# Kernel tuning notes

Hardware: AMD Instinct MI355X
Metric: run time of the kernel (lower is better)

The kernel has to match this reference:

```python
import jax, jax.numpy as jnp
import numpy as np

N_VARS = 100
MAX_LAG = 10
HIDDEN = 64
E = N_VARS * MAX_LAG  # number of tiny expert MLPs
BATCH = 4096


def setup_inputs() -> dict:
    key = jax.random.key(0)
    k_x, k_w1, k_b1, k_w2, k_b2 = jax.random.split(key, 5)
    x = jax.random.normal(k_x, (BATCH, E), dtype=jnp.float32)
    # PyTorch Linear(1, H): weight [H,1] -> stacked as [E, H]; bias [E, H]
    lim1 = 1.0  # kaiming-uniform-ish bound for fan_in=1
    W1 = jax.random.uniform(k_w1, (E, HIDDEN), dtype=jnp.float32, minval=-lim1, maxval=lim1)
    b1 = jax.random.uniform(k_b1, (E, HIDDEN), dtype=jnp.float32, minval=-lim1, maxval=lim1)
    # Linear(H, n_vars): weight [n_vars,H] -> stacked as [E, H, n_vars]; bias [E, n_vars]
    lim2 = 1.0 / np.sqrt(HIDDEN)
    W2 = jax.random.uniform(k_w2, (E, HIDDEN, N_VARS), dtype=jnp.float32, minval=-lim2, maxval=lim2)
    b2 = jax.random.uniform(k_b2, (E, N_VARS), dtype=jnp.float32, minval=-lim2, maxval=lim2)
    return {"x": x, "W1": W1, "b1": b1, "W2": W2, "b2": b2}


def reference(x, W1, b1, W2, b2):
    # Fused form of: sum_i Linear2_i(relu(Linear1_i(x[:, i:i+1])))
    # h[b,e,h] = relu(x[b,e] * W1[e,h] + b1[e,h])
    h = jax.nn.relu(x[:, :, None] * W1[None, :, :] + b1[None, :, :])  # [B,E,H]
    # sum over experts folded into the contraction: out[b,v] = sum_e h[b,e,:] @ W2[e,:,v]
    out = jnp.einsum("beh,ehv->bv", h, W2) + jnp.sum(b2, axis=0)  # [B,n_vars]
    return out
```

## Files before the change

kernel.cpp:

```cpp
#include <hip/hip_runtime.h>
#include <hip/hip_bf16.h>

#define NV 100
#define HID 64
#define NE 1000
#define NB 4096
#define ESPLIT 32
#define W2E 3584

typedef __attribute__((ext_vector_type(8))) short short8;
typedef __attribute__((ext_vector_type(4))) float f32x4;

__device__ __align__(16) float g_bsum[NV];

__device__ __forceinline__ short cvtbf(float f) {
    return __builtin_bit_cast(short, (__bf16)f);
}
__device__ __forceinline__ unsigned short f2bf(float f) {
    return (unsigned short)__builtin_bit_cast(short, (__bf16)f);
}
__device__ __forceinline__ float bf2f(unsigned short s) {
    union { unsigned u; float f; } v; v.u = ((unsigned)s) << 16;
    return v.f;
}
__device__ __forceinline__ unsigned pkbf(float a, float b) {
    return (unsigned)f2bf(a) | ((unsigned)f2bf(b) << 16);
}

__device__ __host__ __forceinline__ void esplit_range(int ks, int* pe0, int* pne) {
    int e0 = (ks < 26) ? 32 * ks : 832 + 28 * (ks - 26);
    int ne = (ks < 26) ? 32 : 28;
    *pe0 = e0; *pne = ne;
}

__global__ void bias_kernel(const float* __restrict__ b2) {
    int v = blockIdx.x;
    float s = 0.f;
    for (int e = threadIdx.x; e < NE; e += 256)
        s += b2[e * NV + v];
    __shared__ float red[4];
    for (int off = 32; off; off >>= 1) s += __shfl_down(s, off, 64);
    if ((threadIdx.x & 63) == 0) red[threadIdx.x >> 6] = s;
    __syncthreads();
    if (threadIdx.x == 0) g_bsum[v] = red[0] + red[1] + red[2] + red[3];
}

__global__ void init_kernel(float* __restrict__ out) {
    int idx = blockIdx.x * 256 + threadIdx.x;
    if (idx < NB * NV) out[idx] = g_bsum[idx % NV];
}

__global__ void prepass3(const float* __restrict__ W2, unsigned* __restrict__ w2bf) {
    __shared__ float t[HID][NV + 1];
    int e = blockIdx.x;
    const float* src = W2 + (size_t)e * (HID * NV);
    for (int i = threadIdx.x; i < HID * NV; i += 256) {
        int hh = i / NV;
        int v = i - hh * NV;
        t[hh][v] = src[i];
    }
    __syncthreads();
    unsigned* dst = w2bf + (size_t)e * W2E;
    for (int o = threadIdx.x; o < W2E; o += 256) {
        int f = o >> 8;
        int r = o & 255;
        int l = r >> 2;
        int q = r & 3;
        int ksh = f / 7, tt = f - 7 * ksh;
        int kg = l >> 4, lrow = l & 15;
        int h0 = ksh * 32 + kg * 8 + 2 * q;
        int v = tt * 16 + lrow;
        unsigned val = 0;
        if (v < NV) val = pkbf(t[h0][v], t[h0 + 1][v]);
        dst[o] = val;
    }
}

__global__ __launch_bounds__(256, 2) void moe5(
    const float* __restrict__ x, const float* __restrict__ W1,
    const float* __restrict__ b1, const unsigned* __restrict__ w2bf,
    float* __restrict__ part)
{
    __shared__ __align__(16) unsigned char smem[61440];
    unsigned short* xts = (unsigned short*)(smem + 28672);
    float* w1l = (float*)(smem + 45056);
    float* b1l = (float*)(smem + 53248);

    const int bid = blockIdx.x;
    const int xcd = bid & 7;
    const int jj  = bid >> 3;
    const int ks  = xcd * 4 + (jj & 3);
    const int mb  = jj >> 2;

    const int tid  = threadIdx.x;
    const int lane = tid & 63;
    const int wave = tid >> 6;
    const int lrow = lane & 15;
    const int kg   = lane >> 4;

    const int row0 = mb * 256;
    int e0, ne; esplit_range(ks, &e0, &ne);

    {
        const float* xp = x + (size_t)(row0 + tid) * NE + e0;
        #pragma unroll
        for (int c4 = 0; c4 < 8; ++c4) {
            int eb = c4 * 4;
            if (eb < ne) {
                float4 v = *(const float4*)(xp + eb);
                xts[(eb + 0) * 256 + tid] = f2bf(v.x);
                xts[(eb + 1) * 256 + tid] = f2bf(v.y);
                xts[(eb + 2) * 256 + tid] = f2bf(v.z);
                xts[(eb + 3) * 256 + tid] = f2bf(v.w);
            }
        }
    }
    {
        int e = tid >> 3;
        int h = (tid & 7) * 8;
        if (e < ne) {
            const float* wsrc = W1 + (size_t)(e0 + e) * HID + h;
            const float* bsrc = b1 + (size_t)(e0 + e) * HID + h;
            *(float4*)&w1l[e * 64 + h]     = *(const float4*)(wsrc);
            *(float4*)&w1l[e * 64 + h + 4] = *(const float4*)(wsrc + 4);
            *(float4*)&b1l[e * 64 + h]     = *(const float4*)(bsrc);
            *(float4*)&b1l[e * 64 + h + 4] = *(const float4*)(bsrc + 4);
        }
    }

    auto stage_w2 = [&](int buf, int e) {
        const unsigned* g = w2bf + (size_t)e * W2E;
        unsigned* lbase = (unsigned*)(smem + buf * 14336);
        #pragma unroll
        for (int k = 0; k < 3; ++k) {
            int off16 = k * 256 + tid;
            __builtin_amdgcn_global_load_lds(
                (const __attribute__((address_space(1))) unsigned*)(g + off16 * 4),
                (__attribute__((address_space(3))) unsigned*)(lbase + off16 * 4),
                16, 0, 0);
        }
        if (tid < 128)
            __builtin_amdgcn_global_load_lds(
                (const __attribute__((address_space(1))) unsigned*)(g + (768 + tid) * 4),
                (__attribute__((address_space(3))) unsigned*)(lbase + (768 + tid) * 4),
                16, 0, 0);
    };

    stage_w2(0, e0);
    __syncthreads();

    f32x4 acc[4][7];
    #pragma unroll
    for (int rf = 0; rf < 4; ++rf)
        #pragma unroll
        for (int t = 0; t < 7; ++t)
            acc[rf][t] = (f32x4){0.f, 0.f, 0.f, 0.f};

    int cur = 0;
    for (int ei = 0; ei < ne; ++ei) {
        if (ei + 1 < ne) stage_w2(cur ^ 1, e0 + ei + 1);

        float xv[4];
        #pragma unroll
        for (int rf = 0; rf < 4; ++rf)
            xv[rf] = bf2f(xts[ei * 256 + wave * 64 + rf * 16 + lrow]);

        const unsigned char* w2c = smem + cur * 14336 + lane * 16;

        #pragma unroll
        for (int ksh = 0; ksh < 2; ++ksh) {
            const int hb = ksh * 32 + kg * 8;
            float4 wa = *(const float4*)&w1l[ei * 64 + hb];
            float4 wb = *(const float4*)&w1l[ei * 64 + hb + 4];
            float4 ba = *(const float4*)&b1l[ei * 64 + hb];
            float4 bb = *(const float4*)&b1l[ei * 64 + hb + 4];

            short8 afr[4];
            #pragma unroll
            for (int rf = 0; rf < 4; ++rf) {
                float xr = xv[rf];
                short8 a;
                a[0] = cvtbf(fmaxf(fmaf(xr, wa.x, ba.x), 0.f));
                a[1] = cvtbf(fmaxf(fmaf(xr, wa.y, ba.y), 0.f));
                a[2] = cvtbf(fmaxf(fmaf(xr, wa.z, ba.z), 0.f));
                a[3] = cvtbf(fmaxf(fmaf(xr, wa.w, ba.w), 0.f));
                a[4] = cvtbf(fmaxf(fmaf(xr, wb.x, bb.x), 0.f));
                a[5] = cvtbf(fmaxf(fmaf(xr, wb.y, bb.y), 0.f));
                a[6] = cvtbf(fmaxf(fmaf(xr, wb.z, bb.z), 0.f));
                a[7] = cvtbf(fmaxf(fmaf(xr, wb.w, bb.w), 0.f));
                afr[rf] = a;
            }

            #pragma unroll
            for (int t = 0; t < 7; ++t) {
                short8 bf = *(const short8*)(w2c + ((ksh * 7 + t) << 10));
                #pragma unroll
                for (int rf = 0; rf < 4; ++rf)
                    acc[rf][t] = __builtin_amdgcn_mfma_f32_16x16x32_bf16(afr[rf], bf, acc[rf][t], 0, 0, 0);
            }
        }
        __syncthreads();
        cur ^= 1;
    }

    float* dst = part + (size_t)ks * (NB * NV);
    #pragma unroll
    for (int rf = 0; rf < 4; ++rf) {
        #pragma unroll
        for (int t = 0; t < 7; ++t) {
            int col = t * 16 + lrow;
            if (col < NV) {
                size_t base = (size_t)(row0 + wave * 64 + rf * 16 + kg * 4) * NV + col;
                #pragma unroll
                for (int r = 0; r < 4; ++r)
                    dst[base + (size_t)r * NV] = acc[rf][t][r];
            }
        }
    }
}

__global__ void reduce2(const float* __restrict__ part, float* __restrict__ out) {
    int i4 = blockIdx.x * 256 + threadIdx.x;
    f32x4 s = *(const f32x4*)&g_bsum[(i4 % 25) * 4];
    size_t off = (size_t)i4 * 4;
    #pragma unroll 4
    for (int k = 0; k < ESPLIT; ++k)
        s += *(const f32x4*)&part[(size_t)k * (NB * NV) + off];
    *(f32x4*)&out[off] = s;
}

#define LDW 72
__global__ __launch_bounds__(256, 3) void moe_fallback(
    const float* __restrict__ x, const float* __restrict__ W1,
    const float* __restrict__ b1, const float* __restrict__ W2,
    float* __restrict__ dst)
{
    __shared__ unsigned short w2t[8192];
    const int tid  = threadIdx.x;
    const int lane = tid & 63;
    const int wave = tid >> 6;
    const int lrow = lane & 15;
    const int kg   = lane >> 4;
    const int row0 = blockIdx.x * 128 + wave * 32;
    const int e0 = blockIdx.y * 32;
    const int e1 = min(NE, e0 + 32);

    f32x4 acc[2][7];
    #pragma unroll
    for (int rf = 0; rf < 2; ++rf)
        #pragma unroll
        for (int t = 0; t < 7; ++t)
            acc[rf][t] = (f32x4){0.f, 0.f, 0.f, 0.f};

    const float* xr0 = x + (size_t)(row0 + lrow) * NE;
    const float* xr1 = x + (size_t)(row0 + 16 + lrow) * NE;

    for (int e = e0; e < e1; ++e) {
        __syncthreads();
        const float* src = W2 + (size_t)e * (HID * NV);
        unsigned* w2t32 = (unsigned*)w2t;
        #pragma unroll
        for (int k = 0; k < 13; ++k) {
            int i = tid + k * 256;
            if (i < (HID / 2) * NV) {
                int a3  = i / 400;
                int rem = i - a3 * 400;
                int bv  = rem >> 2;
                int c   = rem & 3;
                int hh2 = a3 * 4 + c;
                float f0 = src[(2 * hh2) * NV + bv];
                float f1 = src[(2 * hh2 + 1) * NV + bv];
                w2t32[bv * (LDW / 2) + hh2] = pkbf(f0, f1);
            }
        }
        __syncthreads();

        float xv0 = xr0[e];
        float xv1 = xr1[e];
        const float* w1p = W1 + e * HID;
        const float* b1p = b1 + e * HID;
        #pragma unroll
        for (int ksh = 0; ksh < 2; ++ksh) {
            const int hb = ksh * 32 + kg * 8;
            f32x4 w1lo = *(const f32x4*)(w1p + hb);
            f32x4 w1hi = *(const f32x4*)(w1p + hb + 4);
            f32x4 blo  = *(const f32x4*)(b1p + hb);
            f32x4 bhi  = *(const f32x4*)(b1p + hb + 4);
            short8 a0, a1;
            #pragma unroll
            for (int j = 0; j < 4; ++j) {
                a0[j]     = cvtbf(fmaxf(fmaf(xv0, w1lo[j], blo[j]), 0.f));
                a0[j + 4] = cvtbf(fmaxf(fmaf(xv0, w1hi[j], bhi[j]), 0.f));
                a1[j]     = cvtbf(fmaxf(fmaf(xv1, w1lo[j], blo[j]), 0.f));
                a1[j + 4] = cvtbf(fmaxf(fmaf(xv1, w1hi[j], bhi[j]), 0.f));
            }
            #pragma unroll
            for (int t = 0; t < 7; ++t) {
                short8 bf = *(const short8*)&w2t[(t * 16 + lrow) * LDW + hb];
                acc[0][t] = __builtin_amdgcn_mfma_f32_16x16x32_bf16(a0, bf, acc[0][t], 0, 0, 0);
                acc[1][t] = __builtin_amdgcn_mfma_f32_16x16x32_bf16(a1, bf, acc[1][t], 0, 0, 0);
            }
        }
    }

    #pragma unroll
    for (int rf = 0; rf < 2; ++rf) {
        #pragma unroll
        for (int t = 0; t < 7; ++t) {
            int col = t * 16 + lrow;
            if (col < NV) {
                size_t base = (size_t)(row0 + rf * 16 + kg * 4) * NV + col;
                #pragma unroll
                for (int r = 0; r < 4; ++r)
                    atomicAdd(&dst[base + (size_t)r * NV], acc[rf][t][r]);
            }
        }
    }
}

extern "C" void kernel_launch(void* const* d_in, const int* in_sizes, int n_in,
                              void* d_out, int out_size, void* d_ws, size_t ws_size,
                              hipStream_t stream) {
    const float* x  = (const float*)d_in[0];
    const float* W1 = (const float*)d_in[1];
    const float* b1 = (const float*)d_in[2];
    const float* W2 = (const float*)d_in[3];
    const float* b2 = (const float*)d_in[4];
    float* out = (float*)d_out;

    const size_t W2BF_BYTES = (size_t)NE * W2E * 4;
    const size_t PART_BYTES = (size_t)ESPLIT * NB * NV * 4;

    bias_kernel<<<NV, 256, 0, stream>>>(b2);

    if (ws_size >= W2BF_BYTES + PART_BYTES) {
        unsigned* w2bf = (unsigned*)d_ws;
        float* part = (float*)((char*)d_ws + W2BF_BYTES);
        prepass3<<<NE, 256, 0, stream>>>(W2, w2bf);
        moe5<<<512, 256, 0, stream>>>(x, W1, b1, w2bf, part);
        reduce2<<<(NB * NV / 4 + 255) / 256, 256, 0, stream>>>(part, out);
    } else {
        init_kernel<<<(NB * NV + 255) / 256, 256, 0, stream>>>(out);
        moe_fallback<<<dim3(NB / 128, ESPLIT), 256, 0, stream>>>(x, W1, b1, W2, out);
    }
}
```

Before: 83.96 us.

## Pack W1/b1 with W2 per expert and triple-buffer staging

After: 86.74 us. +3.3%, slower.

```diff
diff --git a/kernel.cpp b/kernel.cpp
--- a/kernel.cpp
+++ b/kernel.cpp
@@ -6,7 +6,7 @@
 #define NE 1000
 #define NB 4096
 #define ESPLIT 32
-#define W2E 3584
+#define BLOB 4096
 
 typedef __attribute__((ext_vector_type(8))) short short8;
 typedef __attribute__((ext_vector_type(4))) float f32x4;
@@ -50,7 +50,8 @@
     if (idx < NB * NV) out[idx] = g_bsum[idx % NV];
 }
 
-__global__ void prepass3(const float* __restrict__ W2, unsigned* __restrict__ w2bf) {
+__global__ void prepass4(const float* __restrict__ W2, const float* __restrict__ W1,
+                         const float* __restrict__ b1, unsigned* __restrict__ blob) {
     __shared__ float t[HID][NV + 1];
     int e = blockIdx.x;
     const float* src = W2 + (size_t)e * (HID * NV);
@@ -60,8 +61,8 @@
         t[hh][v] = src[i];
     }
     __syncthreads();
-    unsigned* dst = w2bf + (size_t)e * W2E;
-    for (int o = threadIdx.x; o < W2E; o += 256) {
+    unsigned* dst = blob + (size_t)e * BLOB;
+    for (int o = threadIdx.x; o < 3584; o += 256) {
         int f = o >> 8;
         int r = o & 255;
         int l = r >> 2;
@@ -74,17 +75,18 @@
         if (v < NV) val = pkbf(t[h0][v], t[h0 + 1][v]);
         dst[o] = val;
     }
-}
-
-__global__ __launch_bounds__(256, 2) void moe5(
-    const float* __restrict__ x, const float* __restrict__ W1,
-    const float* __restrict__ b1, const unsigned* __restrict__ w2bf,
+    if (threadIdx.x < 64) {
+        dst[3584 + threadIdx.x] = __builtin_bit_cast(unsigned, W1[(size_t)e * HID + threadIdx.x]);
+        dst[3648 + threadIdx.x] = __builtin_bit_cast(unsigned, b1[(size_t)e * HID + threadIdx.x]);
+    }
+}
+
+__global__ __launch_bounds__(256, 2) void moe7(
+    const float* __restrict__ x, const unsigned* __restrict__ blob,
     float* __restrict__ part)
 {
-    __shared__ __align__(16) unsigned char smem[61440];
-    unsigned short* xts = (unsigned short*)(smem + 28672);
-    float* w1l = (float*)(smem + 45056);
-    float* b1l = (float*)(smem + 53248);
+    __shared__ __align__(16) unsigned char smem[65536];
+    unsigned short* xts = (unsigned short*)(smem + 49152);
 
     const int bid = blockIdx.x;
     const int xcd = bid & 7;
@@ -101,6 +103,21 @@
     const int row0 = mb * 256;
     int e0, ne; esplit_range(ks, &e0, &ne);
 
+    auto stage = [&](int buf, int e) {
+        const unsigned* g = blob + (size_t)e * BLOB;
+        unsigned* lbase = (unsigned*)(smem + buf * 16384);
+        #pragma unroll
+        for (int k = 0; k < 4; ++k) {
+            int off = (k * 256 + tid) * 4;
+            __builtin_amdgcn_global_load_lds(
+                (const __attribute__((address_space(1))) unsigned*)(g + off),
+                (__attribute__((address_space(3))) unsigned*)(lbase + off),
+                16, 0, 0);
+        }
+    };
+
+    stage(0, e0);
+    stage(1, e0 + 1);
     {
         const float* xp = x + (size_t)(row0 + tid) * NE + e0;
         #pragma unroll
@@ -115,38 +132,6 @@
             }
         }
     }
-    {
-        int e = tid >> 3;
-        int h = (tid & 7) * 8;
-        if (e < ne) {
-            const float* wsrc = W1 + (size_t)(e0 + e) * HID + h;
-            const float* bsrc = b1 + (size_t)(e0 + e) * HID + h;
-            *(float4*)&w1l[e * 64 + h]     = *(const float4*)(wsrc);
-            *(float4*)&w1l[e * 64 + h + 4] = *(const float4*)(wsrc + 4);
-            *(float4*)&b1l[e * 64 + h]     = *(const float4*)(bsrc);
-            *(float4*)&b1l[e * 64 + h + 4] = *(const float4*)(bsrc + 4);
-        }
-    }
-
-    auto stage_w2 = [&](int buf, int e) {
-        const unsigned* g = w2bf + (size_t)e * W2E;
-        unsigned* lbase = (unsigned*)(smem + buf * 14336);
-        #pragma unroll
-        for (int k = 0; k < 3; ++k) {
-            int off16 = k * 256 + tid;
-            __builtin_amdgcn_global_load_lds(
-                (const __attribute__((address_space(1))) unsigned*)(g + off16 * 4),
-                (__attribute__((address_space(3))) unsigned*)(lbase + off16 * 4),
-                16, 0, 0);
-        }
-        if (tid < 128)
-            __builtin_amdgcn_global_load_lds(
-                (const __attribute__((address_space(1))) unsigned*)(g + (768 + tid) * 4),
-                (__attribute__((address_space(3))) unsigned*)(lbase + (768 + tid) * 4),
-                16, 0, 0);
-    };
-
-    stage_w2(0, e0);
     __syncthreads();
 
     f32x4 acc[4][7];
@@ -156,24 +141,33 @@
         for (int t = 0; t < 7; ++t)
             acc[rf][t] = (f32x4){0.f, 0.f, 0.f, 0.f};
 
-    int cur = 0;
+    int bi = 0;
     for (int ei = 0; ei < ne; ++ei) {
-        if (ei + 1 < ne) stage_w2(cur ^ 1, e0 + ei + 1);
+        asm volatile("s_waitcnt vmcnt(4)" ::: "memory");
+        __builtin_amdgcn_s_barrier();
+        __builtin_amdgcn_sched_barrier(0);
+
+        if (ei + 2 < ne) {
+            int b2 = bi + 2; if (b2 >= 3) b2 -= 3;
+            stage(b2, e0 + ei + 2);
+        }
+
+        const unsigned char* buf = smem + bi * 16384;
+        const float* w1p = (const float*)(buf + 14336);
+        const float* b1p = (const float*)(buf + 14592);
 
         float xv[4];
         #pragma unroll
         for (int rf = 0; rf < 4; ++rf)
             xv[rf] = bf2f(xts[ei * 256 + wave * 64 + rf * 16 + lrow]);
 
-        const unsigned char* w2c = smem + cur * 14336 + lane * 16;
-
         #pragma unroll
         for (int ksh = 0; ksh < 2; ++ksh) {
             const int hb = ksh * 32 + kg * 8;
-            float4 wa = *(const float4*)&w1l[ei * 64 + hb];
-            float4 wb = *(const float4*)&w1l[ei * 64 + hb + 4];
-            float4 ba = *(const float4*)&b1l[ei * 64 + hb];
-            float4 bb = *(const float4*)&b1l[ei * 64 + hb + 4];
+            float4 wa = *(const float4*)(w1p + hb);
+            float4 wb = *(const float4*)(w1p + hb + 4);
+            float4 ba = *(const float4*)(b1p + hb);
+            float4 bb = *(const float4*)(b1p + hb + 4);
 
             short8 afr[4];
             #pragma unroll
@@ -191,16 +185,18 @@
                 afr[rf] = a;
             }
 
+            __builtin_amdgcn_s_setprio(1);
             #pragma unroll
             for (int t = 0; t < 7; ++t) {
-                short8 bf = *(const short8*)(w2c + ((ksh * 7 + t) << 10));
+                short8 bf = *(const short8*)(buf + ((ksh * 7 + t) << 10) + lane * 16);
                 #pragma unroll
                 for (int rf = 0; rf < 4; ++rf)
                     acc[rf][t] = __builtin_amdgcn_mfma_f32_16x16x32_bf16(afr[rf], bf, acc[rf][t], 0, 0, 0);
             }
-        }
-        __syncthreads();
-        cur ^= 1;
+            __builtin_amdgcn_s_setprio(0);
+        }
+        __builtin_amdgcn_sched_barrier(0);
+        bi = (bi + 1 == 3) ? 0 : bi + 1;
     }
 
     float* dst = part + (size_t)ks * (NB * NV);
@@ -238,9 +234,9 @@
     __shared__ unsigned short w2t[8192];
     const int tid  = threadIdx.x;
     const int lane = tid & 63;
-    const int wave = tid >> 6;
     const int lrow = lane & 15;
     const int kg   = lane >> 4;
+    const int wave = tid >> 6;
     const int row0 = blockIdx.x * 128 + wave * 32;
     const int e0 = blockIdx.y * 32;
     const int e1 = min(NE, e0 + 32);
@@ -328,16 +324,16 @@
     const float* b2 = (const float*)d_in[4];
     float* out = (float*)d_out;
 
-    const size_t W2BF_BYTES = (size_t)NE * W2E * 4;
+    const size_t BLOB_BYTES = (size_t)NE * BLOB * 4;
     const size_t PART_BYTES = (size_t)ESPLIT * NB * NV * 4;
 
     bias_kernel<<<NV, 256, 0, stream>>>(b2);
 
-    if (ws_size >= W2BF_BYTES + PART_BYTES) {
-        unsigned* w2bf = (unsigned*)d_ws;
-        float* part = (float*)((char*)d_ws + W2BF_BYTES);
-        prepass3<<<NE, 256, 0, stream>>>(W2, w2bf);
-        moe5<<<512, 256, 0, stream>>>(x, W1, b1, w2bf, part);
+    if (ws_size >= BLOB_BYTES + PART_BYTES) {
+        unsigned* blob = (unsigned*)d_ws;
+        float* part = (float*)((char*)d_ws + BLOB_BYTES);
+        prepass4<<<NE, 256, 0, stream>>>(W2, W1, b1, blob);
+        moe7<<<512, 256, 0, stream>>>(x, blob, part);
         reduce2<<<(NB * NV / 4 + 255) / 256, 256, 0, stream>>>(part, out);
     } else {
         init_kernel<<<(NB * NV + 255) / 256, 256, 0, stream>>>(out);
```
